# Kernel optimization log

Measured on AMD Instinct MI355X. Metric: run time of the kernel, lower is better.

The kernel has to match this reference:

```python
import jax, jax.numpy as jnp
import numpy as np

DIM = 1024
NUM_HEADS = 16
HEAD_DIM = DIM // NUM_HEADS
SCALE = HEAD_DIM ** -0.5
HIDDEN = int(DIM * 1.0)


def setup_inputs() -> dict:
    key = jax.random.key(0)
    ks = jax.random.split(key, 11)
    s = 0.02
    return {
        "x":  jax.random.normal(ks[0], (2, 2048, DIM), jnp.float32),
        "Wq": jax.random.normal(ks[1], (DIM, DIM), jnp.float32) * s,
        "bq": jnp.zeros((DIM,), jnp.float32),
        "Wk": jax.random.normal(ks[2], (DIM, DIM), jnp.float32) * s,
        "bk": jnp.zeros((DIM,), jnp.float32),
        "Wv": jax.random.normal(ks[3], (DIM, DIM), jnp.float32) * s,
        "bv": jnp.zeros((DIM,), jnp.float32),
        "W1": jax.random.normal(ks[4], (HIDDEN, DIM), jnp.float32) * s,
        "b1": jnp.zeros((HIDDEN,), jnp.float32),
        "W2": jax.random.normal(ks[5], (DIM, HIDDEN), jnp.float32) * s,
        "b2": jnp.zeros((DIM,), jnp.float32),
    }


def _split_heads(t, B, S):
    # [B,S,C] -> [B,H,S,hd]
    return t.reshape(B, S, NUM_HEADS, HEAD_DIM).transpose(0, 2, 1, 3)


def reference(x, Wq, bq, Wk, bk, Wv, bv, W1, b1, W2, b2):
    B, S, C = x.shape
    q = _split_heads(x @ Wq.T + bq, B, S) * SCALE
    k = _split_heads(x @ Wk.T + bk, B, S)
    v = _split_heads(x @ Wv.T + bv, B, S)
    # softmax-free bilinear attention, scores in float32 (matches .float())
    attn = jnp.einsum('bhqd,bhkd->bhqk', q.astype(jnp.float32), k.astype(jnp.float32))
    out = jnp.einsum('bhqk,bhkd->bhqd', attn, v)  # [B,H,S,hd]
    out = out.transpose(0, 2, 1, 3).reshape(B, S, C)
    h = jax.nn.gelu(out @ W1.T + b1, approximate=False)
    mlp = h @ W2.T + b2
    return x + out + mlp
```

## Files before the change

### kernel.cpp

```cpp
#include <hip/hip_runtime.h>
#include <math.h>

#define DIM    1024
#define BATCH  2
#define SEQ    2048
#define NHEAD  16
#define HDIM   64
#define MROWS  (BATCH*SEQ)
#define NSPLIT 8

typedef unsigned short u16;
typedef __attribute__((ext_vector_type(8))) short  s16x8;
typedef __attribute__((ext_vector_type(4))) float  f32x4;

__device__ __forceinline__ float bf2f(u16 h) {
    unsigned u = ((unsigned)h) << 16; float f; __builtin_memcpy(&f, &u, 4); return f;
}
__device__ __forceinline__ u16 f2bf(float f) {
    unsigned u; __builtin_memcpy(&u, &f, 4);
    u += 0x7FFFu + ((u >> 16) & 1u);
    return (u16)(u >> 16);
}

__global__ __launch_bounds__(256)
void pack_all(const float* __restrict__ x,
              const float* __restrict__ Wq, const float* __restrict__ Wk,
              const float* __restrict__ Wv, const float* __restrict__ W1,
              const float* __restrict__ W2,
              u16* __restrict__ xb, u16* __restrict__ Wqb, u16* __restrict__ Wkb,
              u16* __restrict__ Wvb, u16* __restrict__ W1b, u16* __restrict__ W2b)
{
    const int bid = blockIdx.x;
    const float* src; u16* dst; int i;
    if (bid < 4096) { src = x; dst = xb; i = bid * 256 + threadIdx.x; }
    else {
        const int w = (bid - 4096) >> 10;
        const int lb = (bid - 4096) & 1023;
        src = (w == 0) ? Wq : (w == 1) ? Wk : (w == 2) ? Wv : (w == 3) ? W1 : W2;
        dst = (w == 0) ? Wqb : (w == 1) ? Wkb : (w == 2) ? Wvb : (w == 3) ? W1b : W2b;
        i = lb * 256 + threadIdx.x;
    }
    float4 v = ((const float4*)src)[i];
    ushort4 o = { f2bf(v.x), f2bf(v.y), f2bf(v.z), f2bf(v.w) };
    ((ushort4*)dst)[i] = o;
}

__device__ __forceinline__ void gemm_core_pf128(const u16* __restrict__ Ab,
                                                const u16* __restrict__ Bb,
                                                u16* As, u16* Bs,
                                                int tid, f32x4 acc[4][4])
{
    const int w = tid >> 6, l = tid & 63;
    const int wm = (w >> 1) * 64, wn = (w & 1) * 64;
    const int lr = l & 15, kq = l >> 4;
    const int row = tid >> 2, cg8 = (tid & 3) * 8;

    const u16* a0 = Ab + (size_t)row * DIM + cg8;
    const u16* a1 = Ab + (size_t)(64 + row) * DIM + cg8;
    const u16* b0 = Bb + (size_t)row * DIM + cg8;
    const u16* b1 = Bb + (size_t)(64 + row) * DIM + cg8;

    uint4 pa0 = *(const uint4*)a0, pa1 = *(const uint4*)a1;
    uint4 pb0 = *(const uint4*)b0, pb1 = *(const uint4*)b1;
    *(uint4*)(As + tid * 8) = pa0;  *(uint4*)(As + 2048 + tid * 8) = pa1;
    *(uint4*)(Bs + tid * 8) = pb0;  *(uint4*)(Bs + 2048 + tid * 8) = pb1;

    const int NIT = DIM / 32;
    for (int it = 0; it < NIT; ++it) {
        u16* Ac = As + (it & 1) * 4096;
        u16* Bc = Bs + (it & 1) * 4096;
        __syncthreads();
        if (it + 1 < NIT) {
            const int k = (it + 1) * 32;
            pa0 = *(const uint4*)(a0 + k); pa1 = *(const uint4*)(a1 + k);
            pb0 = *(const uint4*)(b0 + k); pb1 = *(const uint4*)(b1 + k);
        }
        s16x8 af[4], bfr[4];
        #pragma unroll
        for (int i = 0; i < 4; ++i)
            af[i]  = *(const s16x8*)(Ac + (wm + i * 16 + lr) * 32 + kq * 8);
        #pragma unroll
        for (int j = 0; j < 4; ++j)
            bfr[j] = *(const s16x8*)(Bc + (wn + j * 16 + lr) * 32 + kq * 8);
        #pragma unroll
        for (int i = 0; i < 4; ++i)
            #pragma unroll
            for (int j = 0; j < 4; ++j)
                acc[i][j] = __builtin_amdgcn_mfma_f32_16x16x32_bf16(af[i], bfr[j], acc[i][j], 0, 0, 0);
        if (it + 1 < NIT) {
            u16* An = As + ((it + 1) & 1) * 4096;
            u16* Bn = Bs + ((it + 1) & 1) * 4096;
            *(uint4*)(An + tid * 8) = pa0;  *(uint4*)(An + 2048 + tid * 8) = pa1;
            *(uint4*)(Bn + tid * 8) = pb0;  *(uint4*)(Bn + 2048 + tid * 8) = pb1;
        }
    }
}

__device__ __forceinline__ void gemm_core_pf64(const u16* __restrict__ Ab,
                                               const u16* __restrict__ Bb,
                                               u16* As , u16* Bs ,
                                               int tid, f32x4 acc[2][4])
{
    const int w  = tid >> 6, l = tid & 63;
    const int wm = (w >> 1) * 32, wn = (w & 1) * 64;
    const int lr = l & 15, kq = l >> 4;
    const int row = tid >> 2, cg8 = (tid & 3) * 8;

    const u16* a0 = Ab + (size_t)row * DIM + cg8;
    const u16* b0 = Bb + (size_t)row * DIM + cg8;
    const u16* b1 = Bb + (size_t)(64 + row) * DIM + cg8;

    uint4 pa  = *(const uint4*)a0;
    uint4 pb0 = *(const uint4*)b0, pb1 = *(const uint4*)b1;
    *(uint4*)(As + tid * 8) = pa;
    *(uint4*)(Bs + tid * 8) = pb0; *(uint4*)(Bs + 2048 + tid * 8) = pb1;

    const int NIT = DIM / 32;
    for (int it = 0; it < NIT; ++it) {
        u16* Ac = As + (it & 1) * 2048;
        u16* Bc = Bs + (it & 1) * 4096;
        __syncthreads();
        if (it + 1 < NIT) {
            const int k = (it + 1) * 32;
            pa  = *(const uint4*)(a0 + k);
            pb0 = *(const uint4*)(b0 + k); pb1 = *(const uint4*)(b1 + k);
        }
        s16x8 af[2], bfr[4];
        #pragma unroll
        for (int i = 0; i < 2; ++i)
            af[i]  = *(const s16x8*)(Ac + (wm + i * 16 + lr) * 32 + kq * 8);
        #pragma unroll
        for (int j = 0; j < 4; ++j)
            bfr[j] = *(const s16x8*)(Bc + (wn + j * 16 + lr) * 32 + kq * 8);
        #pragma unroll
        for (int i = 0; i < 2; ++i)
            #pragma unroll
            for (int j = 0; j < 4; ++j)
                acc[i][j] = __builtin_amdgcn_mfma_f32_16x16x32_bf16(af[i], bfr[j], acc[i][j], 0, 0, 0);
        if (it + 1 < NIT) {
            u16* An = As + ((it + 1) & 1) * 2048;
            u16* Bn = Bs + ((it + 1) & 1) * 4096;
            *(uint4*)(An + tid * 8) = pa;
            *(uint4*)(Bn + tid * 8) = pb0; *(uint4*)(Bn + 2048 + tid * 8) = pb1;
        }
    }
}

__global__ __launch_bounds__(256)
void qkv_gemm(const u16* __restrict__ xb,
              const u16* __restrict__ Wq, const u16* __restrict__ Wk, const u16* __restrict__ Wv,
              const float* __restrict__ bq, const float* __restrict__ bk, const float* __restrict__ bv,
              u16* __restrict__ qo, u16* __restrict__ ko, u16* __restrict__ vo)
{
    __shared__ u16 As[2 * 4096];
    __shared__ u16 Bs[2 * 4096];
    const int tid = threadIdx.x;
    const int m0  = blockIdx.x * 128;
    const int sel = blockIdx.y >> 3;
    const int n0  = (blockIdx.y & 7) * 128;
    const u16*   B    = (sel == 0) ? Wq : (sel == 1) ? Wk : Wv;
    const float* bias = (sel == 0) ? bq : (sel == 1) ? bk : bv;
    u16*         C    = (sel == 0) ? qo : (sel == 1) ? ko : vo;
    const float scale = (sel == 0) ? 0.125f : 1.0f;

    f32x4 acc[4][4];
    #pragma unroll
    for (int i = 0; i < 4; ++i)
        #pragma unroll
        for (int j = 0; j < 4; ++j) acc[i][j] = (f32x4){0.f, 0.f, 0.f, 0.f};

    gemm_core_pf128(xb + (size_t)m0 * DIM, B + (size_t)n0 * DIM, As, Bs, tid, acc);

    const int w = tid >> 6, l = tid & 63;
    const int wm = (w >> 1) * 64, wn = (w & 1) * 64;
    const int er = l >> 4, ec = l & 15;
    #pragma unroll
    for (int j = 0; j < 4; ++j) {
        const int n = n0 + wn + j * 16 + ec;
        const float bb = bias[n];
        #pragma unroll
        for (int i = 0; i < 4; ++i)
            #pragma unroll
            for (int r = 0; r < 4; ++r) {
                const int m = m0 + wm + i * 16 + er * 4 + r;
                C[(size_t)m * DIM + n] = f2bf((acc[i][j][r] + bb) * scale);
            }
    }
}

__global__ __launch_bounds__(256)
void gemm_bf16(const u16* __restrict__ A, const u16* __restrict__ B,
               const float* __restrict__ bias,
               u16* __restrict__ Cb, float* __restrict__ Cf,
               const float* __restrict__ rx, const u16* __restrict__ rattn,
               int mode)
{
    __shared__ u16 As[2 * 2048];
    __shared__ u16 Bs[2 * 4096];
    const int tid = threadIdx.x;
    const int m0 = blockIdx.x * 64, n0 = blockIdx.y * 128;

    f32x4 acc[2][4];
    #pragma unroll
    for (int i = 0; i < 2; ++i)
        #pragma unroll
        for (int j = 0; j < 4; ++j) acc[i][j] = (f32x4){0.f, 0.f, 0.f, 0.f};

    gemm_core_pf64(A + (size_t)m0 * DIM, B + (size_t)n0 * DIM, As, Bs, tid, acc);

    const int w = tid >> 6, l = tid & 63;
    const int wm = (w >> 1) * 32, wn = (w & 1) * 64;
    const int er = l >> 4, ec = l & 15;
    #pragma unroll
    for (int j = 0; j < 4; ++j) {
        const int n = n0 + wn + j * 16 + ec;
        const float bb = bias[n];
        #pragma unroll
        for (int i = 0; i < 2; ++i)
            #pragma unroll
            for (int r = 0; r < 4; ++r) {
                const int m = m0 + wm + i * 16 + er * 4 + r;
                const size_t idx = (size_t)m * DIM + n;
                float v = acc[i][j][r] + bb;
                if (mode == 1) {
                    v = 0.5f * v * (1.0f + erff(v * 0.70710678118654752f));
                    Cb[idx] = f2bf(v);
                } else {
                    Cf[idx] = v + rx[idx] + bf2f(rattn[idx]);
                }
            }
    }
}

__global__ __launch_bounds__(256)
void ktv_mfma(const u16* __restrict__ Kb, const u16* __restrict__ Vb,
              float* __restrict__ part)
{
    __shared__ u16 Kt[64 * 264];
    __shared__ u16 Vt[64 * 264];
    const int tid = threadIdx.x;
    const int bh = blockIdx.x & 31;
    const int sp = blockIdx.x >> 5;
    const int b = bh >> 4, h = bh & 15;
    const size_t base = (size_t)b * SEQ * DIM + (size_t)h * HDIM + (size_t)sp * 256 * DIM;

    const int dg = (tid & 15) * 4;
    #pragma unroll
    for (int pass = 0; pass < 16; ++pass) {
        const int s = (tid >> 4) + 16 * pass;
        ushort4 kv = *(const ushort4*)(Kb + base + (size_t)s * DIM + dg);
        ushort4 vv = *(const ushort4*)(Vb + base + (size_t)s * DIM + dg);
        Kt[(dg + 0) * 264 + s] = kv.x; Kt[(dg + 1) * 264 + s] = kv.y;
        Kt[(dg + 2) * 264 + s] = kv.z; Kt[(dg + 3) * 264 + s] = kv.w;
        Vt[(dg + 0) * 264 + s] = vv.x; Vt[(dg + 1) * 264 + s] = vv.y;
        Vt[(dg + 2) * 264 + s] = vv.z; Vt[(dg + 3) * 264 + s] = vv.w;
    }
    __syncthreads();

    const int w = tid >> 6, l = tid & 63;
    const int lr = l & 15, kq = l >> 4;
    f32x4 acc[4];
    #pragma unroll
    for (int j = 0; j < 4; ++j) acc[j] = (f32x4){0.f, 0.f, 0.f, 0.f};

    for (int k0 = 0; k0 < 256; k0 += 32) {
        s16x8 af = *(const s16x8*)(Kt + (w * 16 + lr) * 264 + k0 + kq * 8);
        #pragma unroll
        for (int j = 0; j < 4; ++j) {
            s16x8 bf = *(const s16x8*)(Vt + (j * 16 + lr) * 264 + k0 + kq * 8);
            acc[j] = __builtin_amdgcn_mfma_f32_16x16x32_bf16(af, bf, acc[j], 0, 0, 0);
        }
    }

    float* dst = part + ((size_t)sp * 32 + bh) * (HDIM * HDIM);
    const int er = l >> 4, ec = l & 15;
    #pragma unroll
    for (int j = 0; j < 4; ++j)
        #pragma unroll
        for (int r = 0; r < 4; ++r)
            dst[(w * 16 + er * 4 + r) * HDIM + j * 16 + ec] = acc[j][r];
}

__global__ __launch_bounds__(256)
void qktv_kernel(const u16* __restrict__ Qb, const float* __restrict__ part,
                 u16* __restrict__ attnb)
{
    __shared__ float KV[HDIM * HDIM];
    __shared__ u16 Qs[128 * 68];
    const int tid = threadIdx.x;
    const int h  = blockIdx.x;
    const int mt = blockIdx.y;
    const int row0 = mt * 128;
    const int b = row0 >> 11;
    const int bh = b * NHEAD + h;

    for (int i = tid; i < HDIM * HDIM; i += 256) {
        float s = 0.f;
        #pragma unroll
        for (int sp = 0; sp < NSPLIT; ++sp)
            s += part[((size_t)sp * 32 + bh) * (HDIM * HDIM) + i];
        KV[i] = s;
    }
    const int dg = (tid & 15) * 4;
    #pragma unroll
    for (int pass = 0; pass < 8; ++pass) {
        const int r = (tid >> 4) + 16 * pass;
        ushort4 q = *(const ushort4*)(Qb + (size_t)(row0 + r) * DIM + h * HDIM + dg);
        *(ushort4*)(Qs + r * 68 + dg) = q;
    }
    __syncthreads();

    const int tr = tid >> 3, tc = tid & 7;
    const int r0 = tr * 4, c0 = tc * 8;
    float acc[4][8] = {};
    for (int d = 0; d < HDIM; ++d) {
        float4 ka  = *(const float4*)&KV[d * HDIM + c0];
        float4 kb2 = *(const float4*)&KV[d * HDIM + c0 + 4];
        const float* k8a = (const float*)&ka;
        const float* k8b = (const float*)&kb2;
        float qv[4];
        #pragma unroll
        for (int i = 0; i < 4; ++i) qv[i] = bf2f(Qs[(r0 + i) * 68 + d]);
        #pragma unroll
        for (int i = 0; i < 4; ++i)
            #pragma unroll
            for (int j = 0; j < 4; ++j) {
                acc[i][j]     += qv[i] * k8a[j];
                acc[i][j + 4] += qv[i] * k8b[j];
            }
    }
    #pragma unroll
    for (int i = 0; i < 4; ++i) {
        u16* dst = attnb + (size_t)(row0 + r0 + i) * DIM + h * HDIM + c0;
        ushort4 o0 = { f2bf(acc[i][0]), f2bf(acc[i][1]), f2bf(acc[i][2]), f2bf(acc[i][3]) };
        ushort4 o1 = { f2bf(acc[i][4]), f2bf(acc[i][5]), f2bf(acc[i][6]), f2bf(acc[i][7]) };
        *(ushort4*)(dst)     = o0;
        *(ushort4*)(dst + 4) = o1;
    }
}

extern "C" void kernel_launch(void* const* d_in, const int* in_sizes, int n_in,
                              void* d_out, int out_size, void* d_ws, size_t ws_size,
                              hipStream_t stream)
{
    const float* x  = (const float*)d_in[0];
    const float* Wq = (const float*)d_in[1];
    const float* bq = (const float*)d_in[2];
    const float* Wk = (const float*)d_in[3];
    const float* bk = (const float*)d_in[4];
    const float* Wv = (const float*)d_in[5];
    const float* bv = (const float*)d_in[6];
    const float* W1 = (const float*)d_in[7];
    const float* b1 = (const float*)d_in[8];
    const float* W2 = (const float*)d_in[9];
    const float* b2 = (const float*)d_in[10];
    float* out = (float*)d_out;

    char* ws = (char*)d_ws;
    const size_t MB = 1u << 20;
    u16* xb   = (u16*)(ws);
    u16* Wqb  = (u16*)(ws +  8 * MB);
    u16* Wkb  = (u16*)(ws + 10 * MB);
    u16* Wvb  = (u16*)(ws + 12 * MB);
    u16* W1b  = (u16*)(ws + 14 * MB);
    u16* W2b  = (u16*)(ws + 16 * MB);
    u16* qb   = (u16*)(ws + 18 * MB);
    u16* kb   = (u16*)(ws + 26 * MB);
    u16* vb   = (u16*)(ws + 34 * MB);
    float* part = (float*)(ws + 42 * MB);
    u16* attnb = kb;
    u16* h1b   = vb;

    pack_all<<<4096 + 5 * 1024, 256, 0, stream>>>(x, Wq, Wk, Wv, W1, W2,
                                                  xb, Wqb, Wkb, Wvb, W1b, W2b);

    qkv_gemm<<<dim3(32, 24), 256, 0, stream>>>(xb, Wqb, Wkb, Wvb, bq, bk, bv, qb, kb, vb);

    ktv_mfma<<<NSPLIT * 32, 256, 0, stream>>>(kb, vb, part);
    qktv_kernel<<<dim3(NHEAD, MROWS / 128), 256, 0, stream>>>(qb, part, attnb);

    gemm_bf16<<<dim3(64, 8), 256, 0, stream>>>(attnb, W1b, b1, h1b, nullptr, nullptr, nullptr, 1);
    gemm_bf16<<<dim3(64, 8), 256, 0, stream>>>(h1b, W2b, b2, nullptr, out, x, attnb, 2);
}
```

Baseline: 203.7 us.

## Fuse W1/W2 bf16 conversion into MLP GEMM loads and enlarge MLP tiles

The MLP GEMMs now read the fp32 W1/W2 weights directly and convert them to bf16 while staging into shared memory, so the pack kernel no longer converts those two matrices. The MLP GEMM tile grows from 64x128 to 128x128 with a 4x4 accumulator, and the grid order is swapped in the QKV and MLP launches so that blocks sharing the same A rows run next to each other. This removes a conversion pass and its extra traffic, at the cost of twice the B load bandwidth per tile, conversion work inside the K loop, and half as many blocks (256) for the MLP GEMMs.

```diff
diff --git a/kernel.cpp b/kernel.cpp
--- a/kernel.cpp
+++ b/kernel.cpp
@@ -1,4 +1,5 @@
 #include <hip/hip_runtime.h>
+#include <hip/hip_bf16.h>
 #include <math.h>
 
 #define DIM    1024
@@ -21,14 +22,23 @@
     u += 0x7FFFu + ((u >> 16) & 1u);
     return (u16)(u >> 16);
 }
+__device__ __forceinline__ unsigned pack_bf2(float a, float b) {
+    __hip_bfloat162 h2 = __float22bfloat162_rn(float2{a, b});
+    unsigned r; __builtin_memcpy(&r, &h2, 4); return r;
+}
+__device__ __forceinline__ uint4 cvt8(float4 lo, float4 hi) {
+    uint4 r;
+    r.x = pack_bf2(lo.x, lo.y); r.y = pack_bf2(lo.z, lo.w);
+    r.z = pack_bf2(hi.x, hi.y); r.w = pack_bf2(hi.z, hi.w);
+    return r;
+}
 
 __global__ __launch_bounds__(256)
 void pack_all(const float* __restrict__ x,
               const float* __restrict__ Wq, const float* __restrict__ Wk,
-              const float* __restrict__ Wv, const float* __restrict__ W1,
-              const float* __restrict__ W2,
+              const float* __restrict__ Wv,
               u16* __restrict__ xb, u16* __restrict__ Wqb, u16* __restrict__ Wkb,
-              u16* __restrict__ Wvb, u16* __restrict__ W1b, u16* __restrict__ W2b)
+              u16* __restrict__ Wvb)
 {
     const int bid = blockIdx.x;
     const float* src; u16* dst; int i;
@@ -36,8 +46,8 @@
     else {
         const int w = (bid - 4096) >> 10;
         const int lb = (bid - 4096) & 1023;
-        src = (w == 0) ? Wq : (w == 1) ? Wk : (w == 2) ? Wv : (w == 3) ? W1 : W2;
-        dst = (w == 0) ? Wqb : (w == 1) ? Wkb : (w == 2) ? Wvb : (w == 3) ? W1b : W2b;
+        src = (w == 0) ? Wq : (w == 1) ? Wk : Wv;
+        dst = (w == 0) ? Wqb : (w == 1) ? Wkb : Wvb;
         i = lb * 256 + threadIdx.x;
     }
     float4 v = ((const float4*)src)[i];
@@ -96,52 +106,57 @@
     }
 }
 
-__device__ __forceinline__ void gemm_core_pf64(const u16* __restrict__ Ab,
-                                               const u16* __restrict__ Bb,
-                                               u16* As , u16* Bs ,
-                                               int tid, f32x4 acc[2][4])
-{
-    const int w  = tid >> 6, l = tid & 63;
-    const int wm = (w >> 1) * 32, wn = (w & 1) * 64;
+__device__ __forceinline__ void gemm_core_pf128_a16b32(const u16* __restrict__ Ab,
+                                                       const float* __restrict__ Bf,
+                                                       u16* As, u16* Bs,
+                                                       int tid, f32x4 acc[4][4])
+{
+    const int w = tid >> 6, l = tid & 63;
+    const int wm = (w >> 1) * 64, wn = (w & 1) * 64;
     const int lr = l & 15, kq = l >> 4;
     const int row = tid >> 2, cg8 = (tid & 3) * 8;
 
-    const u16* a0 = Ab + (size_t)row * DIM + cg8;
-    const u16* b0 = Bb + (size_t)row * DIM + cg8;
-    const u16* b1 = Bb + (size_t)(64 + row) * DIM + cg8;
-
-    uint4 pa  = *(const uint4*)a0;
-    uint4 pb0 = *(const uint4*)b0, pb1 = *(const uint4*)b1;
-    *(uint4*)(As + tid * 8) = pa;
-    *(uint4*)(Bs + tid * 8) = pb0; *(uint4*)(Bs + 2048 + tid * 8) = pb1;
+    const u16*   a0 = Ab + (size_t)row * DIM + cg8;
+    const u16*   a1 = Ab + (size_t)(64 + row) * DIM + cg8;
+    const float* b0 = Bf + (size_t)row * DIM + cg8;
+    const float* b1 = Bf + (size_t)(64 + row) * DIM + cg8;
+
+    uint4 pa0 = *(const uint4*)a0, pa1 = *(const uint4*)a1;
+    float4 q00 = *(const float4*)b0, q01 = *(const float4*)(b0 + 4);
+    float4 q10 = *(const float4*)b1, q11 = *(const float4*)(b1 + 4);
+    *(uint4*)(As + tid * 8) = pa0;  *(uint4*)(As + 2048 + tid * 8) = pa1;
+    *(uint4*)(Bs + tid * 8) = cvt8(q00, q01);
+    *(uint4*)(Bs + 2048 + tid * 8) = cvt8(q10, q11);
 
     const int NIT = DIM / 32;
     for (int it = 0; it < NIT; ++it) {
-        u16* Ac = As + (it & 1) * 2048;
+        u16* Ac = As + (it & 1) * 4096;
         u16* Bc = Bs + (it & 1) * 4096;
         __syncthreads();
         if (it + 1 < NIT) {
             const int k = (it + 1) * 32;
-            pa  = *(const uint4*)(a0 + k);
-            pb0 = *(const uint4*)(b0 + k); pb1 = *(const uint4*)(b1 + k);
-        }
-        s16x8 af[2], bfr[4];
-        #pragma unroll
-        for (int i = 0; i < 2; ++i)
+            pa0 = *(const uint4*)(a0 + k); pa1 = *(const uint4*)(a1 + k);
+            q00 = *(const float4*)(b0 + k); q01 = *(const float4*)(b0 + k + 4);
+            q10 = *(const float4*)(b1 + k); q11 = *(const float4*)(b1 + k + 4);
+        }
+        s16x8 af[4], bfr[4];
+        #pragma unroll
+        for (int i = 0; i < 4; ++i)
             af[i]  = *(const s16x8*)(Ac + (wm + i * 16 + lr) * 32 + kq * 8);
         #pragma unroll
         for (int j = 0; j < 4; ++j)
             bfr[j] = *(const s16x8*)(Bc + (wn + j * 16 + lr) * 32 + kq * 8);
         #pragma unroll
-        for (int i = 0; i < 2; ++i)
+        for (int i = 0; i < 4; ++i)
             #pragma unroll
             for (int j = 0; j < 4; ++j)
                 acc[i][j] = __builtin_amdgcn_mfma_f32_16x16x32_bf16(af[i], bfr[j], acc[i][j], 0, 0, 0);
         if (it + 1 < NIT) {
-            u16* An = As + ((it + 1) & 1) * 2048;
+            u16* An = As + ((it + 1) & 1) * 4096;
             u16* Bn = Bs + ((it + 1) & 1) * 4096;
-            *(uint4*)(An + tid * 8) = pa;
-            *(uint4*)(Bn + tid * 8) = pb0; *(uint4*)(Bn + 2048 + tid * 8) = pb1;
+            *(uint4*)(An + tid * 8) = pa0;  *(uint4*)(An + 2048 + tid * 8) = pa1;
+            *(uint4*)(Bn + tid * 8) = cvt8(q00, q01);
+            *(uint4*)(Bn + 2048 + tid * 8) = cvt8(q10, q11);
         }
     }
 }
@@ -155,9 +170,9 @@
     __shared__ u16 As[2 * 4096];
     __shared__ u16 Bs[2 * 4096];
     const int tid = threadIdx.x;
-    const int m0  = blockIdx.x * 128;
-    const int sel = blockIdx.y >> 3;
-    const int n0  = (blockIdx.y & 7) * 128;
+    const int sel = blockIdx.x >> 3;
+    const int n0  = (blockIdx.x & 7) * 128;
+    const int m0  = blockIdx.y * 128;
     const u16*   B    = (sel == 0) ? Wq : (sel == 1) ? Wk : Wv;
     const float* bias = (sel == 0) ? bq : (sel == 1) ? bk : bv;
     u16*         C    = (sel == 0) ? qo : (sel == 1) ? ko : vo;
@@ -189,34 +204,34 @@
 }
 
 __global__ __launch_bounds__(256)
-void gemm_bf16(const u16* __restrict__ A, const u16* __restrict__ B,
-               const float* __restrict__ bias,
-               u16* __restrict__ Cb, float* __restrict__ Cf,
-               const float* __restrict__ rx, const u16* __restrict__ rattn,
-               int mode)
-{
-    __shared__ u16 As[2 * 2048];
+void gemm_mlp(const u16* __restrict__ A, const float* __restrict__ Bf,
+              const float* __restrict__ bias,
+              u16* __restrict__ Cb, float* __restrict__ Cf,
+              const float* __restrict__ rx, const u16* __restrict__ rattn,
+              int mode)
+{
+    __shared__ u16 As[2 * 4096];
     __shared__ u16 Bs[2 * 4096];
     const int tid = threadIdx.x;
-    const int m0 = blockIdx.x * 64, n0 = blockIdx.y * 128;
-
-    f32x4 acc[2][4];
-    #pragma unroll
-    for (int i = 0; i < 2; ++i)
+    const int n0 = blockIdx.x * 128, m0 = blockIdx.y * 128;
+
+    f32x4 acc[4][4];
+    #pragma unroll
+    for (int i = 0; i < 4; ++i)
         #pragma unroll
         for (int j = 0; j < 4; ++j) acc[i][j] = (f32x4){0.f, 0.f, 0.f, 0.f};
 
-    gemm_core_pf64(A + (size_t)m0 * DIM, B + (size_t)n0 * DIM, As, Bs, tid, acc);
-
-    const int w = tid >> 6, l = tid & 63;
-    const int wm = (w >> 1) * 32, wn = (w & 1) * 64;
+    gemm_core_pf128_a16b32(A + (size_t)m0 * DIM, Bf + (size_t)n0 * DIM, As, Bs, tid, acc);
+
+    const int w = tid >> 6, l = tid & 63;
+    const int wm = (w >> 1) * 64, wn = (w & 1) * 64;
     const int er = l >> 4, ec = l & 15;
     #pragma unroll
     for (int j = 0; j < 4; ++j) {
         const int n = n0 + wn + j * 16 + ec;
         const float bb = bias[n];
         #pragma unroll
-        for (int i = 0; i < 2; ++i)
+        for (int i = 0; i < 4; ++i)
             #pragma unroll
             for (int r = 0; r < 4; ++r) {
                 const int m = m0 + wm + i * 16 + er * 4 + r;
@@ -362,8 +377,6 @@
     u16* Wqb  = (u16*)(ws +  8 * MB);
     u16* Wkb  = (u16*)(ws + 10 * MB);
     u16* Wvb  = (u16*)(ws + 12 * MB);
-    u16* W1b  = (u16*)(ws + 14 * MB);
-    u16* W2b  = (u16*)(ws + 16 * MB);
     u16* qb   = (u16*)(ws + 18 * MB);
     u16* kb   = (u16*)(ws + 26 * MB);
     u16* vb   = (u16*)(ws + 34 * MB);
@@ -371,14 +384,13 @@
     u16* attnb = kb;
     u16* h1b   = vb;
 
-    pack_all<<<4096 + 5 * 1024, 256, 0, stream>>>(x, Wq, Wk, Wv, W1, W2,
-                                                  xb, Wqb, Wkb, Wvb, W1b, W2b);
-
-    qkv_gemm<<<dim3(32, 24), 256, 0, stream>>>(xb, Wqb, Wkb, Wvb, bq, bk, bv, qb, kb, vb);
+    pack_all<<<4096 + 3 * 1024, 256, 0, stream>>>(x, Wq, Wk, Wv, xb, Wqb, Wkb, Wvb);
+
+    qkv_gemm<<<dim3(24, 32), 256, 0, stream>>>(xb, Wqb, Wkb, Wvb, bq, bk, bv, qb, kb, vb);
 
     ktv_mfma<<<NSPLIT * 32, 256, 0, stream>>>(kb, vb, part);
     qktv_kernel<<<dim3(NHEAD, MROWS / 128), 256, 0, stream>>>(qb, part, attnb);
 
-    gemm_bf16<<<dim3(64, 8), 256, 0, stream>>>(attnb, W1b, b1, h1b, nullptr, nullptr, nullptr, 1);
-    gemm_bf16<<<dim3(64, 8), 256, 0, stream>>>(h1b, W2b, b2, nullptr, out, x, attnb, 2);
-}
+    gemm_mlp<<<dim3(8, 32), 256, 0, stream>>>(attnb, W1, b1, h1b, nullptr, nullptr, nullptr, 1);
+    gemm_mlp<<<dim3(8, 32), 256, 0, stream>>>(h1b, W2, b2, nullptr, out, x, attnb, 2);
+}
```

Result: slower. 233.5 us (+14.6%).

## Fuse x fp32-to-bf16 conversion into QKV GEMM loads and remap block order

Applied to the files above, without the earlier changes.

Drops the separate conversion of x to bf16 in the pack kernel and instead loads fp32 x directly in the QKV GEMM, converting to bf16 on the way into shared memory with packed bf162 conversions. This removes one write and one read of the bf16 copy of x. The GEMM's global A-loads now double in bytes, and x is re-read across 24 column tiles. The QKV grid becomes 1D with a swizzled block-to-tile mapping, meant to group blocks that share A rows and B columns for better L2 reuse.

```diff
diff --git a/kernel.cpp b/kernel.cpp
--- a/kernel.cpp
+++ b/kernel.cpp
@@ -1,4 +1,5 @@
 #include <hip/hip_runtime.h>
+#include <hip/hip_bf16.h>
 #include <math.h>
 
 #define DIM    1024
@@ -21,48 +22,54 @@
     u += 0x7FFFu + ((u >> 16) & 1u);
     return (u16)(u >> 16);
 }
-
-__global__ __launch_bounds__(256)
-void pack_all(const float* __restrict__ x,
-              const float* __restrict__ Wq, const float* __restrict__ Wk,
-              const float* __restrict__ Wv, const float* __restrict__ W1,
-              const float* __restrict__ W2,
-              u16* __restrict__ xb, u16* __restrict__ Wqb, u16* __restrict__ Wkb,
-              u16* __restrict__ Wvb, u16* __restrict__ W1b, u16* __restrict__ W2b)
-{
-    const int bid = blockIdx.x;
-    const float* src; u16* dst; int i;
-    if (bid < 4096) { src = x; dst = xb; i = bid * 256 + threadIdx.x; }
-    else {
-        const int w = (bid - 4096) >> 10;
-        const int lb = (bid - 4096) & 1023;
-        src = (w == 0) ? Wq : (w == 1) ? Wk : (w == 2) ? Wv : (w == 3) ? W1 : W2;
-        dst = (w == 0) ? Wqb : (w == 1) ? Wkb : (w == 2) ? Wvb : (w == 3) ? W1b : W2b;
-        i = lb * 256 + threadIdx.x;
-    }
+__device__ __forceinline__ unsigned pack_bf2(float a, float b) {
+    __hip_bfloat162 h2 = __float22bfloat162_rn(float2{a, b});
+    unsigned r; __builtin_memcpy(&r, &h2, 4); return r;
+}
+__device__ __forceinline__ uint4 cvt8(float4 lo, float4 hi) {
+    uint4 r;
+    r.x = pack_bf2(lo.x, lo.y); r.y = pack_bf2(lo.z, lo.w);
+    r.z = pack_bf2(hi.x, hi.y); r.w = pack_bf2(hi.z, hi.w);
+    return r;
+}
+
+__global__ __launch_bounds__(256)
+void pack5(const float* __restrict__ Wq, const float* __restrict__ Wk,
+           const float* __restrict__ Wv, const float* __restrict__ W1,
+           const float* __restrict__ W2,
+           u16* __restrict__ Wqb, u16* __restrict__ Wkb, u16* __restrict__ Wvb,
+           u16* __restrict__ W1b, u16* __restrict__ W2b)
+{
+    const int w  = blockIdx.x >> 10;
+    const int lb = blockIdx.x & 1023;
+    const float* src = (w == 0) ? Wq : (w == 1) ? Wk : (w == 2) ? Wv : (w == 3) ? W1 : W2;
+    u16*         dst = (w == 0) ? Wqb : (w == 1) ? Wkb : (w == 2) ? Wvb : (w == 3) ? W1b : W2b;
+    const int i = lb * 256 + threadIdx.x;
     float4 v = ((const float4*)src)[i];
     ushort4 o = { f2bf(v.x), f2bf(v.y), f2bf(v.z), f2bf(v.w) };
     ((ushort4*)dst)[i] = o;
 }
 
-__device__ __forceinline__ void gemm_core_pf128(const u16* __restrict__ Ab,
-                                                const u16* __restrict__ Bb,
-                                                u16* As, u16* Bs,
-                                                int tid, f32x4 acc[4][4])
+__device__ __forceinline__ void gemm_core_pf128_a32(const float* __restrict__ Af,
+                                                    const u16* __restrict__ Bb,
+                                                    u16* As, u16* Bs,
+                                                    int tid, f32x4 acc[4][4])
 {
     const int w = tid >> 6, l = tid & 63;
     const int wm = (w >> 1) * 64, wn = (w & 1) * 64;
     const int lr = l & 15, kq = l >> 4;
     const int row = tid >> 2, cg8 = (tid & 3) * 8;
 
-    const u16* a0 = Ab + (size_t)row * DIM + cg8;
-    const u16* a1 = Ab + (size_t)(64 + row) * DIM + cg8;
-    const u16* b0 = Bb + (size_t)row * DIM + cg8;
-    const u16* b1 = Bb + (size_t)(64 + row) * DIM + cg8;
-
-    uint4 pa0 = *(const uint4*)a0, pa1 = *(const uint4*)a1;
+    const float* a0 = Af + (size_t)row * DIM + cg8;
+    const float* a1 = Af + (size_t)(64 + row) * DIM + cg8;
+    const u16*   b0 = Bb + (size_t)row * DIM + cg8;
+    const u16*   b1 = Bb + (size_t)(64 + row) * DIM + cg8;
+
+    float4 qa00 = *(const float4*)a0, qa01 = *(const float4*)(a0 + 4);
+    float4 qa10 = *(const float4*)a1, qa11 = *(const float4*)(a1 + 4);
     uint4 pb0 = *(const uint4*)b0, pb1 = *(const uint4*)b1;
-    *(uint4*)(As + tid * 8) = pa0;  *(uint4*)(As + 2048 + tid * 8) = pa1;
+    *(uint4*)(As + tid * 8) = cvt8(qa00, qa01);
+    *(uint4*)(As + 2048 + tid * 8) = cvt8(qa10, qa11);
     *(uint4*)(Bs + tid * 8) = pb0;  *(uint4*)(Bs + 2048 + tid * 8) = pb1;
 
     const int NIT = DIM / 32;
@@ -72,8 +79,9 @@
         __syncthreads();
         if (it + 1 < NIT) {
             const int k = (it + 1) * 32;
-            pa0 = *(const uint4*)(a0 + k); pa1 = *(const uint4*)(a1 + k);
-            pb0 = *(const uint4*)(b0 + k); pb1 = *(const uint4*)(b1 + k);
+            qa00 = *(const float4*)(a0 + k); qa01 = *(const float4*)(a0 + k + 4);
+            qa10 = *(const float4*)(a1 + k); qa11 = *(const float4*)(a1 + k + 4);
+            pb0 = *(const uint4*)(b0 + k);   pb1 = *(const uint4*)(b1 + k);
         }
         s16x8 af[4], bfr[4];
         #pragma unroll
@@ -90,7 +98,8 @@
         if (it + 1 < NIT) {
             u16* An = As + ((it + 1) & 1) * 4096;
             u16* Bn = Bs + ((it + 1) & 1) * 4096;
-            *(uint4*)(An + tid * 8) = pa0;  *(uint4*)(An + 2048 + tid * 8) = pa1;
+            *(uint4*)(An + tid * 8) = cvt8(qa00, qa01);
+            *(uint4*)(An + 2048 + tid * 8) = cvt8(qa10, qa11);
             *(uint4*)(Bn + tid * 8) = pb0;  *(uint4*)(Bn + 2048 + tid * 8) = pb1;
         }
     }
@@ -147,7 +156,7 @@
 }
 
 __global__ __launch_bounds__(256)
-void qkv_gemm(const u16* __restrict__ xb,
+void qkv_gemm(const float* __restrict__ xf,
               const u16* __restrict__ Wq, const u16* __restrict__ Wk, const u16* __restrict__ Wv,
               const float* __restrict__ bq, const float* __restrict__ bk, const float* __restrict__ bv,
               u16* __restrict__ qo, u16* __restrict__ ko, u16* __restrict__ vo)
@@ -155,9 +164,12 @@
     __shared__ u16 As[2 * 4096];
     __shared__ u16 Bs[2 * 4096];
     const int tid = threadIdx.x;
-    const int m0  = blockIdx.x * 128;
-    const int sel = blockIdx.y >> 3;
-    const int n0  = (blockIdx.y & 7) * 128;
+    const int id = blockIdx.x;
+    const int k8 = id & 7, j = id >> 3;
+    const int m0 = ((k8 & 3) + 4 * (j & 7)) * 128;
+    const int wsel = (k8 >> 2) * 12 + (j >> 3);
+    const int sel = wsel >> 3;
+    const int n0  = (wsel & 7) * 128;
     const u16*   B    = (sel == 0) ? Wq : (sel == 1) ? Wk : Wv;
     const float* bias = (sel == 0) ? bq : (sel == 1) ? bk : bv;
     u16*         C    = (sel == 0) ? qo : (sel == 1) ? ko : vo;
@@ -167,23 +179,23 @@
     #pragma unroll
     for (int i = 0; i < 4; ++i)
         #pragma unroll
-        for (int j = 0; j < 4; ++j) acc[i][j] = (f32x4){0.f, 0.f, 0.f, 0.f};
-
-    gemm_core_pf128(xb + (size_t)m0 * DIM, B + (size_t)n0 * DIM, As, Bs, tid, acc);
+        for (int jj = 0; jj < 4; ++jj) acc[i][jj] = (f32x4){0.f, 0.f, 0.f, 0.f};
+
+    gemm_core_pf128_a32(xf + (size_t)m0 * DIM, B + (size_t)n0 * DIM, As, Bs, tid, acc);
 
     const int w = tid >> 6, l = tid & 63;
     const int wm = (w >> 1) * 64, wn = (w & 1) * 64;
     const int er = l >> 4, ec = l & 15;
     #pragma unroll
-    for (int j = 0; j < 4; ++j) {
-        const int n = n0 + wn + j * 16 + ec;
+    for (int jj = 0; jj < 4; ++jj) {
+        const int n = n0 + wn + jj * 16 + ec;
         const float bb = bias[n];
         #pragma unroll
         for (int i = 0; i < 4; ++i)
             #pragma unroll
             for (int r = 0; r < 4; ++r) {
                 const int m = m0 + wm + i * 16 + er * 4 + r;
-                C[(size_t)m * DIM + n] = f2bf((acc[i][j][r] + bb) * scale);
+                C[(size_t)m * DIM + n] = f2bf((acc[i][jj][r] + bb) * scale);
             }
     }
 }
@@ -358,23 +370,21 @@
 
     char* ws = (char*)d_ws;
     const size_t MB = 1u << 20;
-    u16* xb   = (u16*)(ws);
-    u16* Wqb  = (u16*)(ws +  8 * MB);
-    u16* Wkb  = (u16*)(ws + 10 * MB);
-    u16* Wvb  = (u16*)(ws + 12 * MB);
-    u16* W1b  = (u16*)(ws + 14 * MB);
-    u16* W2b  = (u16*)(ws + 16 * MB);
-    u16* qb   = (u16*)(ws + 18 * MB);
-    u16* kb   = (u16*)(ws + 26 * MB);
-    u16* vb   = (u16*)(ws + 34 * MB);
-    float* part = (float*)(ws + 42 * MB);
+    u16* Wqb  = (u16*)(ws);
+    u16* Wkb  = (u16*)(ws +  2 * MB);
+    u16* Wvb  = (u16*)(ws +  4 * MB);
+    u16* W1b  = (u16*)(ws +  6 * MB);
+    u16* W2b  = (u16*)(ws +  8 * MB);
+    u16* qb   = (u16*)(ws + 10 * MB);
+    u16* kb   = (u16*)(ws + 18 * MB);
+    u16* vb   = (u16*)(ws + 26 * MB);
+    float* part = (float*)(ws + 34 * MB);
     u16* attnb = kb;
     u16* h1b   = vb;
 
-    pack_all<<<4096 + 5 * 1024, 256, 0, stream>>>(x, Wq, Wk, Wv, W1, W2,
-                                                  xb, Wqb, Wkb, Wvb, W1b, W2b);
-
-    qkv_gemm<<<dim3(32, 24), 256, 0, stream>>>(xb, Wqb, Wkb, Wvb, bq, bk, bv, qb, kb, vb);
+    pack5<<<5 * 1024, 256, 0, stream>>>(Wq, Wk, Wv, W1, W2, Wqb, Wkb, Wvb, W1b, W2b);
+
+    qkv_gemm<<<768, 256, 0, stream>>>(x, Wqb, Wkb, Wvb, bq, bk, bv, qb, kb, vb);
 
     ktv_mfma<<<NSPLIT * 32, 256, 0, stream>>>(kb, vb, part);
     qktv_kernel<<<dim3(NHEAD, MROWS / 128), 256, 0, stream>>>(qb, part, attnb);
```

Result: no change. 204.4 us (+0.3%).
